# Optimization experiments

Hardware: AMD Instinct MI355X
Metric: run time of the kernel (lower is better)

The kernel has to match this reference:

```python
import jax, jax.numpy as jnp
import numpy as np

NUM_GRAPHS_N = 64  # number of segments in node_batch
NUM_GRAPHS_L = 64  # number of segments in label_batch


def setup_inputs() -> dict:
    key = jax.random.key(0)
    k1, k2, k3, k4, k5 = jax.random.split(key, 5)
    N, D = 16384, 256
    En, El = 8192, 8192
    h = jax.random.normal(k1, (N, D), dtype=jnp.float32)
    node_edge = jax.random.randint(k2, (2, En), 0, N, dtype=jnp.int64)
    node_batch = jnp.sort(jax.random.randint(k3, (En,), 0, NUM_GRAPHS_N, dtype=jnp.int64))
    label_edge = jax.random.randint(k4, (2, El), 0, N, dtype=jnp.int64)
    label_batch = jnp.sort(jax.random.randint(k5, (El,), 0, NUM_GRAPHS_L, dtype=jnp.int64))
    return {"h": h, "node_edge": node_edge, "node_batch": node_batch,
            "label_edge": label_edge, "label_batch": label_batch}


def _cdist(a, b):
    # Euclidean pairwise distance, grad-safe sqrt.
    sq = (jnp.sum(a * a, -1)[:, None] + jnp.sum(b * b, -1)[None, :]
          - 2.0 * (a @ b.T))
    sq = jnp.maximum(sq, 0.0)
    safe = jnp.where(sq > 0, sq, 1.0)
    return jnp.where(sq > 0, jnp.sqrt(safe), 0.0)


def _seg_max(x, seg, num):  # max over axis 0; empty segments -> 0 like torch_scatter
    m = jax.ops.segment_max(x, seg, num_segments=num)
    return jnp.where(jnp.isfinite(m), m, 0.0)


def _seg_mean(x, seg, num):
    s = jax.ops.segment_sum(x, seg, num_segments=num)
    cnt = jax.ops.segment_sum(jnp.ones((x.shape[0], 1), x.dtype), seg, num_segments=num)
    return s / jnp.maximum(cnt, 1.0)


def reference(h, node_edge, node_batch, label_edge, label_batch):
    ef_n = (h[node_edge[0]] + h[node_edge[1]]) * 0.5   # [En, D]
    ef_l = (h[label_edge[0]] + h[label_edge[1]]) * 0.5  # [El, D]
    M = -_cdist(ef_n, ef_l)                              # [En, El]
    # max over cols by label_batch -> [En, Gl], then mean over rows by node_batch
    out_n = _seg_max(M.T, label_batch, NUM_GRAPHS_L).T   # [En, Gl]
    out_n = _seg_mean(out_n, node_batch, NUM_GRAPHS_N)   # [Gn, Gl]
    # max over rows by node_batch -> [Gn, El], then mean over cols by label_batch
    out_l = _seg_max(M, node_batch, NUM_GRAPHS_N)        # [Gn, El]
    out_l = _seg_mean(out_l.T, label_batch, NUM_GRAPHS_L).T  # [Gn, Gl]
    return (out_n + out_l) * 0.5
```

## Files before the change

kernel.cpp:

```cpp
#include <hip/hip_runtime.h>
#include <hip/hip_bf16.h>
#include <math.h>

#define EN 8192
#define EL 8192
#define D  256
#define NG 64
#define INF_BITS 0x7f800000u

typedef __attribute__((ext_vector_type(8))) short  bf16x8;
typedef __attribute__((ext_vector_type(4))) float  f32x4;

__device__ __forceinline__ unsigned short f2bf(float f) {
    unsigned u = __float_as_uint(f);
    unsigned r = (u + 0x7fffu + ((u >> 16) & 1u)) >> 16;
    return (unsigned short)r;
}

__global__ void prep(const float* __restrict__ h,
                     const int* __restrict__ node_edge,
                     const int* __restrict__ label_edge,
                     unsigned short* __restrict__ efn, float* __restrict__ normN,
                     unsigned short* __restrict__ efl, float* __restrict__ normL,
                     unsigned* __restrict__ inf_buf)
{
    int b = blockIdx.x;
    if (b < 1024) {
        uint4 v = make_uint4(INF_BITS, INF_BITS, INF_BITS, INF_BITS);
        ((uint4*)inf_buf)[b * 256 + threadIdx.x] = v;
        return;
    }
    b -= 1024;
    const int* edges; unsigned short* ef; float* norm;
    if (b < 2048) { edges = node_edge;  ef = efn; norm = normN; }
    else          { b -= 2048; edges = label_edge; ef = efl; norm = normL; }

    int wave = threadIdx.x >> 6;
    int lane = threadIdx.x & 63;
    int e = b * 4 + wave;
    int a  = edges[e];
    int bb = edges[EN + e];
    float4 va = ((const float4*)(h + (size_t)a  * D))[lane];
    float4 vb = ((const float4*)(h + (size_t)bb * D))[lane];
    float4 f;
    f.x = 0.5f * (va.x + vb.x);
    f.y = 0.5f * (va.y + vb.y);
    f.z = 0.5f * (va.z + vb.z);
    f.w = 0.5f * (va.w + vb.w);
    float sq = f.x*f.x + f.y*f.y + f.z*f.z + f.w*f.w;
    ushort4 pk;
    pk.x = f2bf(f.x); pk.y = f2bf(f.y); pk.z = f2bf(f.z); pk.w = f2bf(f.w);
    ((ushort4*)(ef + (size_t)e * D))[lane] = pk;
    #pragma unroll
    for (int off = 1; off < 64; off <<= 1)
        sq += __shfl_xor(sq, off, 64);
    if (lane == 0) norm[e] = sq;
}

__launch_bounds__(256, 4)
__global__ void dist_min(const unsigned short* __restrict__ A,
                         const unsigned short* __restrict__ B,
                         const float* __restrict__ normN,
                         const float* __restrict__ normL,
                         const int* __restrict__ node_batch,
                         const int* __restrict__ label_batch,
                         unsigned* __restrict__ bufN,
                         unsigned* __restrict__ bufL)
{
    __shared__ unsigned short As[128 * 64];
    __shared__ unsigned short Bs[128 * 64];

    const int tid  = threadIdx.x;
    const int lane = tid & 63;
    const int wave = tid >> 6;
    const int quad = lane >> 4;
    const int lc   = lane & 15;
    const int m0   = blockIdx.y * 128;
    const int n0   = blockIdx.x * 128;
    const int wr   = (wave >> 1) * 64;
    const int wc   = (wave & 1) * 64;

    f32x4 acc[4][4];
    #pragma unroll
    for (int i = 0; i < 4; ++i)
        #pragma unroll
        for (int j = 0; j < 4; ++j) {
            f32x4 z = {0.f, 0.f, 0.f, 0.f};
            acc[i][j] = z;
        }

    for (int kt = 0; kt < 4; ++kt) {
        #pragma unroll
        for (int t = 0; t < 4; ++t) {
            int c = t * 256 + tid;
            int row = c >> 3, cc = c & 7;
            int scc = cc ^ (row & 7);
            const unsigned short* gp = A + (size_t)(m0 + row) * D + kt * 64 + scc * 8;
            __builtin_amdgcn_global_load_lds(
                (const __attribute__((address_space(1))) void*)gp,
                (__attribute__((address_space(3))) void*)(As + c * 8), 16, 0, 0);
        }
        #pragma unroll
        for (int t = 0; t < 4; ++t) {
            int c = t * 256 + tid;
            int row = c >> 3, cc = c & 7;
            int scc = cc ^ (row & 7);
            const unsigned short* gp = B + (size_t)(n0 + row) * D + kt * 64 + scc * 8;
            __builtin_amdgcn_global_load_lds(
                (const __attribute__((address_space(1))) void*)gp,
                (__attribute__((address_space(3))) void*)(Bs + c * 8), 16, 0, 0);
        }
        __syncthreads();

        #pragma unroll
        for (int kk = 0; kk < 2; ++kk) {
            bf16x8 af[4], bfv[4];
            #pragma unroll
            for (int mi = 0; mi < 4; ++mi)
                af[mi] = *(const bf16x8*)(As + (wr + mi*16 + lc) * 64
                                             + ((kk*4 + quad) ^ (lc & 7)) * 8);
            #pragma unroll
            for (int ni = 0; ni < 4; ++ni)
                bfv[ni] = *(const bf16x8*)(Bs + (wc + ni*16 + lc) * 64
                                              + ((kk*4 + quad) ^ (lc & 7)) * 8);
            #pragma unroll
            for (int mi = 0; mi < 4; ++mi)
                #pragma unroll
                for (int ni = 0; ni < 4; ++ni)
                    acc[mi][ni] = __builtin_amdgcn_mfma_f32_16x16x32_bf16(
                        af[mi], bfv[ni], acc[mi][ni], 0, 0, 0);
        }
        __syncthreads();
    }

    float nb[4]; int gl[4];
    #pragma unroll
    for (int ni = 0; ni < 4; ++ni) {
        int col = n0 + wc + ni*16 + lc;
        nb[ni] = normL[col];
        gl[ni] = label_batch[col];
    }
    float na[16]; int gr[16];
    #pragma unroll
    for (int mi = 0; mi < 4; ++mi)
        #pragma unroll
        for (int r = 0; r < 4; ++r) {
            int row = m0 + wr + mi*16 + quad*4 + r;
            na[mi*4 + r] = normN[row];
            gr[mi*4 + r] = node_batch[row];
        }

    #pragma unroll
    for (int mi = 0; mi < 4; ++mi)
        #pragma unroll
        for (int ni = 0; ni < 4; ++ni)
            #pragma unroll
            for (int r = 0; r < 4; ++r)
                acc[mi][ni][r] = fmaxf(
                    fmaf(-2.0f, acc[mi][ni][r], na[mi*4 + r] + nb[ni]), 0.0f);

    const float FINF = __uint_as_float(INF_BITS);

    int glo = label_batch[n0 + wc], ghi = label_batch[n0 + wc + 63];
    for (int g = glo; g <= ghi; ++g) {
        bool s0 = (gl[0] == g), s1 = (gl[1] == g), s2 = (gl[2] == g), s3 = (gl[3] == g);
        float rm[16];
        #pragma unroll
        for (int mi = 0; mi < 4; ++mi)
            #pragma unroll
            for (int r = 0; r < 4; ++r) {
                float m = s0 ? acc[mi][0][r] : FINF;
                m = fminf(m, s1 ? acc[mi][1][r] : FINF);
                m = fminf(m, s2 ? acc[mi][2][r] : FINF);
                m = fminf(m, s3 ? acc[mi][3][r] : FINF);
                m = fminf(m, __shfl_xor(m, 1, 64));
                m = fminf(m, __shfl_xor(m, 2, 64));
                m = fminf(m, __shfl_xor(m, 4, 64));
                m = fminf(m, __shfl_xor(m, 8, 64));
                rm[mi*4 + r] = m;
            }
        if (lc == 0) {
            #pragma unroll
            for (int mi = 0; mi < 4; ++mi)
                #pragma unroll
                for (int r = 0; r < 4; ++r) {
                    int row = m0 + wr + mi*16 + quad*4 + r;
                    atomicMin(&bufN[row * NG + g], __float_as_uint(rm[mi*4 + r]));
                }
        }
    }

    int rlo = node_batch[m0 + wr], rhi = node_batch[m0 + wr + 63];
    for (int g = rlo; g <= rhi; ++g) {
        float cm[4];
        #pragma unroll
        for (int ni = 0; ni < 4; ++ni) {
            float m = FINF;
            #pragma unroll
            for (int mi = 0; mi < 4; ++mi)
                #pragma unroll
                for (int r = 0; r < 4; ++r)
                    m = fminf(m, (gr[mi*4 + r] == g) ? acc[mi][ni][r] : FINF);
            m = fminf(m, __shfl_xor(m, 16, 64));
            m = fminf(m, __shfl_xor(m, 32, 64));
            cm[ni] = m;
        }
        if (quad == 0) {
            #pragma unroll
            for (int ni = 0; ni < 4; ++ni) {
                int col = n0 + wc + ni*16 + lc;
                atomicMin(&bufL[g * EL + col], __float_as_uint(cm[ni]));
            }
        }
    }
}

__device__ __forceinline__ int lbound(const int* __restrict__ a, int n, int v) {
    int lo = 0, hi = n;
    while (lo < hi) { int mid = (lo + hi) >> 1; if (a[mid] < v) lo = mid + 1; else hi = mid; }
    return lo;
}

__global__ void finalize(const unsigned* __restrict__ bufN,
                         const unsigned* __restrict__ bufL,
                         const int* __restrict__ node_batch,
                         const int* __restrict__ label_batch,
                         float* __restrict__ out)
{
    __shared__ float sN[NG];
    __shared__ float sL[NG];
    int gn  = blockIdx.x;
    int tid = threadIdx.x;
    if (tid < NG) { sN[tid] = 0.0f; sL[tid] = 0.0f; }
    __syncthreads();

    int ns = lbound(node_batch, EN, gn);
    int ne = lbound(node_batch, EN, gn + 1);

    {
        int t = tid & 63, strip = tid >> 6;
        float acc = 0.0f;
        for (int i = ns + strip; i < ne; i += 4) {
            unsigned b = bufN[i * NG + t];
            if (b != INF_BITS) acc -= sqrtf(__uint_as_float(b));
        }
        atomicAdd(&sN[t], acc);
    }

    for (int j = tid; j < EL; j += 256) {
        unsigned b = bufL[gn * EL + j];
        if (b != INF_BITS) {
            int g = label_batch[j];
            atomicAdd(&sL[g], -sqrtf(__uint_as_float(b)));
        }
    }
    __syncthreads();

    if (tid < NG) {
        int t = tid;
        int cn = ne - ns;
        int ls = lbound(label_batch, EL, t);
        int le = lbound(label_batch, EL, t + 1);
        int cl = le - ls;
        float out_n = sN[t] / (float)(cn > 0 ? cn : 1);
        float out_l = sL[t] / (float)(cl > 0 ? cl : 1);
        out[gn * NG + t] = 0.5f * (out_n + out_l);
    }
}

extern "C" void kernel_launch(void* const* d_in, const int* in_sizes, int n_in,
                              void* d_out, int out_size, void* d_ws, size_t ws_size,
                              hipStream_t stream)
{
    const float* h          = (const float*)d_in[0];
    const int* node_edge    = (const int*)d_in[1];
    const int* node_batch   = (const int*)d_in[2];
    const int* label_edge   = (const int*)d_in[3];
    const int* label_batch  = (const int*)d_in[4];
    float* out = (float*)d_out;

    char* ws = (char*)d_ws;
    unsigned short* efn = (unsigned short*)ws; ws += (size_t)EN * D * 2;
    unsigned short* efl = (unsigned short*)ws; ws += (size_t)EL * D * 2;
    float* normN = (float*)ws;                 ws += (size_t)EN * 4;
    float* normL = (float*)ws;                 ws += (size_t)EL * 4;
    unsigned* bufN = (unsigned*)ws;            ws += (size_t)EN * NG * 4;
    unsigned* bufL = (unsigned*)ws;            ws += (size_t)NG * EL * 4;

    prep<<<5120, 256, 0, stream>>>(h, node_edge, label_edge,
                                   efn, normN, efl, normL, bufN);
    dist_min<<<dim3(EL / 128, EN / 128), 256, 0, stream>>>(
        efn, efl, normN, normL, node_batch, label_batch, bufN, bufL);
    finalize<<<NG, 256, 0, stream>>>(bufN, bufL, node_batch, label_batch, out);
}
```

Before: 208.4 us.

## Use 8 waves per GEMM block and add single-segment fast paths

The distance GEMM block now runs 512 threads (8 waves), each computing a 32x64 subtile instead of 64x64. This halves accumulator registers per wave and raises the number of waves available to hide latency. Both segment-min reductions get a fast path that skips per-group masking when a wave's rows or columns all fall in one segment. Finalize is launched with 1024 threads and its strides are adjusted to match. The risks are fewer MFMAs per LDS fragment load, which lowers reuse, and the launch bound of (512,4) may constrain registers.

```diff
diff --git a/kernel.cpp b/kernel.cpp
--- a/kernel.cpp
+++ b/kernel.cpp
@@ -57,7 +57,7 @@
     if (lane == 0) norm[e] = sq;
 }
 
-__launch_bounds__(256, 4)
+__launch_bounds__(512, 4)
 __global__ void dist_min(const unsigned short* __restrict__ A,
                          const unsigned short* __restrict__ B,
                          const float* __restrict__ normN,
@@ -77,12 +77,12 @@
     const int lc   = lane & 15;
     const int m0   = blockIdx.y * 128;
     const int n0   = blockIdx.x * 128;
-    const int wr   = (wave >> 1) * 64;
+    const int wr   = (wave >> 1) * 32;
     const int wc   = (wave & 1) * 64;
 
-    f32x4 acc[4][4];
-    #pragma unroll
-    for (int i = 0; i < 4; ++i)
+    f32x4 acc[2][4];
+    #pragma unroll
+    for (int i = 0; i < 2; ++i)
         #pragma unroll
         for (int j = 0; j < 4; ++j) {
             f32x4 z = {0.f, 0.f, 0.f, 0.f};
@@ -91,8 +91,8 @@
 
     for (int kt = 0; kt < 4; ++kt) {
         #pragma unroll
-        for (int t = 0; t < 4; ++t) {
-            int c = t * 256 + tid;
+        for (int t = 0; t < 2; ++t) {
+            int c = t * 512 + tid;
             int row = c >> 3, cc = c & 7;
             int scc = cc ^ (row & 7);
             const unsigned short* gp = A + (size_t)(m0 + row) * D + kt * 64 + scc * 8;
@@ -101,8 +101,8 @@
                 (__attribute__((address_space(3))) void*)(As + c * 8), 16, 0, 0);
         }
         #pragma unroll
-        for (int t = 0; t < 4; ++t) {
-            int c = t * 256 + tid;
+        for (int t = 0; t < 2; ++t) {
+            int c = t * 512 + tid;
             int row = c >> 3, cc = c & 7;
             int scc = cc ^ (row & 7);
             const unsigned short* gp = B + (size_t)(n0 + row) * D + kt * 64 + scc * 8;
@@ -114,9 +114,9 @@
 
         #pragma unroll
         for (int kk = 0; kk < 2; ++kk) {
-            bf16x8 af[4], bfv[4];
-            #pragma unroll
-            for (int mi = 0; mi < 4; ++mi)
+            bf16x8 af[2], bfv[4];
+            #pragma unroll
+            for (int mi = 0; mi < 2; ++mi)
                 af[mi] = *(const bf16x8*)(As + (wr + mi*16 + lc) * 64
                                              + ((kk*4 + quad) ^ (lc & 7)) * 8);
             #pragma unroll
@@ -124,7 +124,7 @@
                 bfv[ni] = *(const bf16x8*)(Bs + (wc + ni*16 + lc) * 64
                                               + ((kk*4 + quad) ^ (lc & 7)) * 8);
             #pragma unroll
-            for (int mi = 0; mi < 4; ++mi)
+            for (int mi = 0; mi < 2; ++mi)
                 #pragma unroll
                 for (int ni = 0; ni < 4; ++ni)
                     acc[mi][ni] = __builtin_amdgcn_mfma_f32_16x16x32_bf16(
@@ -140,9 +140,9 @@
         nb[ni] = normL[col];
         gl[ni] = label_batch[col];
     }
-    float na[16]; int gr[16];
-    #pragma unroll
-    for (int mi = 0; mi < 4; ++mi)
+    float na[8]; int gr[8];
+    #pragma unroll
+    for (int mi = 0; mi < 2; ++mi)
         #pragma unroll
         for (int r = 0; r < 4; ++r) {
             int row = m0 + wr + mi*16 + quad*4 + r;
@@ -151,7 +151,7 @@
         }
 
     #pragma unroll
-    for (int mi = 0; mi < 4; ++mi)
+    for (int mi = 0; mi < 2; ++mi)
         #pragma unroll
         for (int ni = 0; ni < 4; ++ni)
             #pragma unroll
@@ -162,17 +162,14 @@
     const float FINF = __uint_as_float(INF_BITS);
 
     int glo = label_batch[n0 + wc], ghi = label_batch[n0 + wc + 63];
-    for (int g = glo; g <= ghi; ++g) {
-        bool s0 = (gl[0] == g), s1 = (gl[1] == g), s2 = (gl[2] == g), s3 = (gl[3] == g);
-        float rm[16];
-        #pragma unroll
-        for (int mi = 0; mi < 4; ++mi)
+    if (glo == ghi) {
+        float rm[8];
+        #pragma unroll
+        for (int mi = 0; mi < 2; ++mi)
             #pragma unroll
             for (int r = 0; r < 4; ++r) {
-                float m = s0 ? acc[mi][0][r] : FINF;
-                m = fminf(m, s1 ? acc[mi][1][r] : FINF);
-                m = fminf(m, s2 ? acc[mi][2][r] : FINF);
-                m = fminf(m, s3 ? acc[mi][3][r] : FINF);
+                float m = fminf(fminf(acc[mi][0][r], acc[mi][1][r]),
+                                fminf(acc[mi][2][r], acc[mi][3][r]));
                 m = fminf(m, __shfl_xor(m, 1, 64));
                 m = fminf(m, __shfl_xor(m, 2, 64));
                 m = fminf(m, __shfl_xor(m, 4, 64));
@@ -181,26 +178,53 @@
             }
         if (lc == 0) {
             #pragma unroll
-            for (int mi = 0; mi < 4; ++mi)
+            for (int mi = 0; mi < 2; ++mi)
                 #pragma unroll
                 for (int r = 0; r < 4; ++r) {
                     int row = m0 + wr + mi*16 + quad*4 + r;
-                    atomicMin(&bufN[row * NG + g], __float_as_uint(rm[mi*4 + r]));
+                    atomicMin(&bufN[row * NG + glo], __float_as_uint(rm[mi*4 + r]));
                 }
         }
-    }
-
-    int rlo = node_batch[m0 + wr], rhi = node_batch[m0 + wr + 63];
-    for (int g = rlo; g <= rhi; ++g) {
+    } else {
+        for (int g = glo; g <= ghi; ++g) {
+            bool s0 = (gl[0] == g), s1 = (gl[1] == g), s2 = (gl[2] == g), s3 = (gl[3] == g);
+            float rm[8];
+            #pragma unroll
+            for (int mi = 0; mi < 2; ++mi)
+                #pragma unroll
+                for (int r = 0; r < 4; ++r) {
+                    float m = s0 ? acc[mi][0][r] : FINF;
+                    m = fminf(m, s1 ? acc[mi][1][r] : FINF);
+                    m = fminf(m, s2 ? acc[mi][2][r] : FINF);
+                    m = fminf(m, s3 ? acc[mi][3][r] : FINF);
+                    m = fminf(m, __shfl_xor(m, 1, 64));
+                    m = fminf(m, __shfl_xor(m, 2, 64));
+                    m = fminf(m, __shfl_xor(m, 4, 64));
+                    m = fminf(m, __shfl_xor(m, 8, 64));
+                    rm[mi*4 + r] = m;
+                }
+            if (lc == 0) {
+                #pragma unroll
+                for (int mi = 0; mi < 2; ++mi)
+                    #pragma unroll
+                    for (int r = 0; r < 4; ++r) {
+                        int row = m0 + wr + mi*16 + quad*4 + r;
+                        atomicMin(&bufN[row * NG + g], __float_as_uint(rm[mi*4 + r]));
+                    }
+            }
+        }
+    }
+
+    int rlo = node_batch[m0 + wr], rhi = node_batch[m0 + wr + 31];
+    if (rlo == rhi) {
         float cm[4];
         #pragma unroll
         for (int ni = 0; ni < 4; ++ni) {
-            float m = FINF;
-            #pragma unroll
-            for (int mi = 0; mi < 4; ++mi)
-                #pragma unroll
-                for (int r = 0; r < 4; ++r)
-                    m = fminf(m, (gr[mi*4 + r] == g) ? acc[mi][ni][r] : FINF);
+            float m = acc[0][ni][0];
+            m = fminf(m, acc[0][ni][1]); m = fminf(m, acc[0][ni][2]);
+            m = fminf(m, acc[0][ni][3]); m = fminf(m, acc[1][ni][0]);
+            m = fminf(m, acc[1][ni][1]); m = fminf(m, acc[1][ni][2]);
+            m = fminf(m, acc[1][ni][3]);
             m = fminf(m, __shfl_xor(m, 16, 64));
             m = fminf(m, __shfl_xor(m, 32, 64));
             cm[ni] = m;
@@ -209,7 +233,30 @@
             #pragma unroll
             for (int ni = 0; ni < 4; ++ni) {
                 int col = n0 + wc + ni*16 + lc;
-                atomicMin(&bufL[g * EL + col], __float_as_uint(cm[ni]));
+                atomicMin(&bufL[rlo * EL + col], __float_as_uint(cm[ni]));
+            }
+        }
+    } else {
+        for (int g = rlo; g <= rhi; ++g) {
+            float cm[4];
+            #pragma unroll
+            for (int ni = 0; ni < 4; ++ni) {
+                float m = FINF;
+                #pragma unroll
+                for (int mi = 0; mi < 2; ++mi)
+                    #pragma unroll
+                    for (int r = 0; r < 4; ++r)
+                        m = fminf(m, (gr[mi*4 + r] == g) ? acc[mi][ni][r] : FINF);
+                m = fminf(m, __shfl_xor(m, 16, 64));
+                m = fminf(m, __shfl_xor(m, 32, 64));
+                cm[ni] = m;
+            }
+            if (quad == 0) {
+                #pragma unroll
+                for (int ni = 0; ni < 4; ++ni) {
+                    int col = n0 + wc + ni*16 + lc;
+                    atomicMin(&bufL[g * EL + col], __float_as_uint(cm[ni]));
+                }
             }
         }
     }
@@ -240,14 +287,14 @@
     {
         int t = tid & 63, strip = tid >> 6;
         float acc = 0.0f;
-        for (int i = ns + strip; i < ne; i += 4) {
+        for (int i = ns + strip; i < ne; i += 16) {
             unsigned b = bufN[i * NG + t];
             if (b != INF_BITS) acc -= sqrtf(__uint_as_float(b));
         }
         atomicAdd(&sN[t], acc);
     }
 
-    for (int j = tid; j < EL; j += 256) {
+    for (int j = tid; j < EL; j += 1024) {
         unsigned b = bufL[gn * EL + j];
         if (b != INF_BITS) {
             int g = label_batch[j];
@@ -289,7 +336,7 @@
 
     prep<<<5120, 256, 0, stream>>>(h, node_edge, label_edge,
                                    efn, normN, efl, normL, bufN);
-    dist_min<<<dim3(EL / 128, EN / 128), 256, 0, stream>>>(
+    dist_min<<<dim3(EL / 128, EN / 128), 512, 0, stream>>>(
         efn, efl, normN, normL, node_batch, label_batch, bufN, bufL);
-    finalize<<<NG, 256, 0, stream>>>(bufN, bufL, node_batch, label_batch, out);
-}
+    finalize<<<NG, 1024, 0, stream>>>(bufN, bufL, node_batch, label_batch, out);
+}
```

After: 186.1 us. -10.7%, faster.
